# Optimization experiments

Measured on AMD Instinct MI355X. Metric: run time of the kernel, lower is better.

Reference implementation:

```python
import jax, jax.numpy as jnp
import numpy as np

E, D, H, T = 8, 1024, 2816, 16384


def setup_inputs() -> dict:
    key = jax.random.key(0)
    k1, k2, k3, k4 = jax.random.split(key, 4)
    x = jax.random.normal(k1, (T, D), dtype=jnp.float32)
    # Params sized per init (w1/w3: [E, H, D], w2: [E, D, H]), trunc-normal-ish scale 0.02
    w1 = 0.02 * jax.random.normal(k2, (E, H, D), dtype=jnp.float32)
    w2 = 0.02 * jax.random.normal(k3, (E, D, H), dtype=jnp.float32)
    w3 = 0.02 * jax.random.normal(k4, (E, H, D), dtype=jnp.float32)
    # Per-expert token counts summing to < T (tail rows are padding, output zeros)
    rng = np.random.default_rng(0)
    props = rng.dirichlet(4.0 * np.ones(E))
    counts = np.floor(props * (T - 64)).astype(np.int32)
    num_tokens_per_expert = jnp.asarray(counts, dtype=jnp.int32)
    return {"x": x, "w1": w1, "w2": w2, "w3": w3,
            "num_tokens_per_expert": num_tokens_per_expert}


def reference(x, w1, w2, w3, num_tokens_per_expert):
    # Tokens are grouped contiguously by expert; grouped GEMM via lax.ragged_dot.
    g = num_tokens_per_expert.astype(jnp.int32)
    # rhs for ragged_dot must be [groups, k, n]
    h1 = jax.lax.ragged_dot(x, jnp.swapaxes(w1, 1, 2), g)   # [T, H] = x @ w1[e].T
    h3 = jax.lax.ragged_dot(x, jnp.swapaxes(w3, 1, 2), g)   # [T, H]
    h = jax.nn.silu(h1) * h3                                # SwiGLU
    out = jax.lax.ragged_dot(h, jnp.swapaxes(w2, 1, 2), g)  # [T, D]
    # Rows beyond sum(counts) are padding -> zeros, matching torch vstack of zeros
    valid = jnp.arange(x.shape[0]) < jnp.sum(g)
    return jnp.where(valid[:, None], out, jnp.zeros((), dtype=out.dtype))
```

## Files before the change

### kernel.cpp

```cpp
#include <hip/hip_runtime.h>

#define NE 8
#define DD 1024
#define HH 2816
#define TT 16384
#define MT (TT / 128 + NE)

constexpr int NJA = MT * (HH / 128);
constexpr int NJB = MT * (DD / 128);

typedef __bf16 bf16;
typedef __bf16 bf16x4 __attribute__((ext_vector_type(4)));
typedef __bf16 bf16x8 __attribute__((ext_vector_type(8)));
typedef float f32x4 __attribute__((ext_vector_type(4)));

constexpr size_t HBUF_E = (size_t)TT * HH;
constexpr size_t XN = (size_t)TT * DD;
constexpr size_t WN = (size_t)NE * HH * DD;
constexpr size_t XB_OFF = HBUF_E * 2;
constexpr size_t W1B_OFF = XB_OFF + XN * 2;
constexpr size_t W3B_OFF = W1B_OFF + WN * 2;

__device__ __forceinline__ void gld16(const void* g, void* l) {
  __builtin_amdgcn_global_load_lds(
      (const __attribute__((address_space(1))) void*)g,
      (__attribute__((address_space(3))) void*)l, 16, 0, 0);
}

__device__ __forceinline__ f32x4 mfma16(bf16x8 a, bf16x8 b, f32x4 c) {
  return __builtin_amdgcn_mfma_f32_16x16x32_bf16(a, b, c, 0, 0, 0);
}

#define BARRIER()                      \
  do {                                 \
    __builtin_amdgcn_s_barrier();      \
    asm volatile("" ::: "memory");     \
  } while (0)

__global__ __launch_bounds__(256) void cvt_bf16_k(const float4* __restrict__ in,
                                                  bf16x4* __restrict__ out, int n4) {
  int i = blockIdx.x * 256 + threadIdx.x;
  if (i < n4) {
    float4 v = in[i];
    bf16x4 o;
    o[0] = (bf16)v.x; o[1] = (bf16)v.y; o[2] = (bf16)v.z; o[3] = (bf16)v.w;
    out[i] = o;
  }
}

struct TileInfo { int e, row0, rv; };
__device__ __forceinline__ TileInfo find_tile(const int* __restrict__ cnts, int t) {
  TileInfo ti; ti.e = -1; ti.row0 = 0; ti.rv = 0;
  int off = 0;
#pragma unroll
  for (int i = 0; i < NE; ++i) {
    int c = cnts[i];
    int tl = (c + 127) >> 7;
    if (ti.e < 0) {
      if (t < tl) {
        ti.e = i;
        ti.row0 = off + (t << 7);
        int rv = c - (t << 7);
        ti.rv = rv > 128 ? 128 : rv;
      } else {
        t -= tl;
      }
    }
    off += c;
  }
  return ti;
}

__global__ __launch_bounds__(512, 2) void swiglu_gemm_k(
    const bf16* __restrict__ x, const bf16* __restrict__ w1,
    const bf16* __restrict__ w3, const int* __restrict__ cnts,
    bf16* __restrict__ hbuf) {
  constexpr int NKT = DD / 64;

  int lin = blockIdx.x;
  lin = (lin & 7) * (NJA / 8) + (lin >> 3);
  const int tile = lin % MT;
  const int n0 = (lin / MT) * 128;
  TileInfo ti = find_tile(cnts, tile);
  if (ti.e < 0) return;

  const bf16* w1e = w1 + (size_t)ti.e * HH * DD;
  const bf16* w3e = w3 + (size_t)ti.e * HH * DD;
  const bf16* xb = x + (size_t)ti.row0 * DD;

  __shared__ bf16 sA[3][128 * 64];
  __shared__ bf16 sB1[3][128 * 64];
  __shared__ bf16 sB3[3][128 * 64];

  const int tid = threadIdx.x;
  const int lane = tid & 63, wave = tid >> 6;
  const int wm = wave >> 2, wn = wave & 3;
  const int lr = lane & 15, lkg = lane >> 4;

  const int r8 = tid >> 3;
  const int csrc = ((tid & 7) ^ (r8 & 7)) << 3;
  const int rvm1 = ti.rv - 1;
  const int ra0 = r8 > rvm1 ? rvm1 : r8;
  const int ra1 = (64 + r8) > rvm1 ? rvm1 : 64 + r8;
  const bf16* gA0 = xb + (size_t)ra0 * DD + csrc;
  const bf16* gA1 = xb + (size_t)ra1 * DD + csrc;
  const bf16* gB1a = w1e + (size_t)(n0 + r8) * DD + csrc;
  const bf16* gB1b = w1e + (size_t)(n0 + 64 + r8) * DD + csrc;
  const bf16* gB3a = w3e + (size_t)(n0 + r8) * DD + csrc;
  const bf16* gB3b = w3e + (size_t)(n0 + 64 + r8) * DD + csrc;
  const int d0 = tid * 8, d1 = 64 * 64 + tid * 8;

#define STAGE_A(kt, bb)                  \
  do {                                   \
    int kk = (kt) * 64;                  \
    gld16(gA0 + kk, &sA[bb][d0]);        \
    gld16(gA1 + kk, &sA[bb][d1]);        \
    gld16(gB1a + kk, &sB1[bb][d0]);      \
    gld16(gB1b + kk, &sB1[bb][d1]);      \
    gld16(gB3a + kk, &sB3[bb][d0]);      \
    gld16(gB3b + kk, &sB3[bb][d1]);      \
  } while (0)

  const int swz = (lkg ^ (lr & 7)) << 4;
  const int aoff = (wm * 64 + lr) * 128 + swz;
  const int boff = (wn * 32 + lr) * 128 + swz;

  f32x4 acc1[4][2], acc3[4][2];
#pragma unroll
  for (int i = 0; i < 4; ++i)
#pragma unroll
    for (int j = 0; j < 2; ++j) {
      acc1[i][j] = f32x4{0.f, 0.f, 0.f, 0.f};
      acc3[i][j] = f32x4{0.f, 0.f, 0.f, 0.f};
    }

  STAGE_A(0, 0);
  STAGE_A(1, 1);
  asm volatile("s_waitcnt vmcnt(6)" ::: "memory");
  BARRIER();

  int cur = 0;
  for (int kt = 0; kt < NKT; ++kt) {
    const bool pf = (kt + 2) < NKT;
    int nxt = cur + 2; if (nxt >= 3) nxt -= 3;
    if (pf) STAGE_A(kt + 2, nxt);

    const char* pA = (const char*)sA[cur];
    const char* pB1 = (const char*)sB1[cur];
    const char* pB3 = (const char*)sB3[cur];
    bf16x8 af[4][2], f1[2][2], f3[2][2];
#pragma unroll
    for (int mt = 0; mt < 4; ++mt)
#pragma unroll
      for (int ks = 0; ks < 2; ++ks)
        af[mt][ks] = *(const bf16x8*)(pA + ((aoff + mt * 2048) ^ (ks << 6)));
#pragma unroll
    for (int nt = 0; nt < 2; ++nt)
#pragma unroll
      for (int ks = 0; ks < 2; ++ks) {
        f1[nt][ks] = *(const bf16x8*)(pB1 + ((boff + nt * 2048) ^ (ks << 6)));
        f3[nt][ks] = *(const bf16x8*)(pB3 + ((boff + nt * 2048) ^ (ks << 6)));
      }
    __builtin_amdgcn_s_setprio(1);
#pragma unroll
    for (int ks = 0; ks < 2; ++ks)
#pragma unroll
      for (int mt = 0; mt < 4; ++mt)
#pragma unroll
        for (int nt = 0; nt < 2; ++nt) {
          acc1[mt][nt] = mfma16(af[mt][ks], f1[nt][ks], acc1[mt][nt]);
          acc3[mt][nt] = mfma16(af[mt][ks], f3[nt][ks], acc3[mt][nt]);
        }
    __builtin_amdgcn_s_setprio(0);
    if (pf) asm volatile("s_waitcnt vmcnt(6) lgkmcnt(0)" ::: "memory");
    else    asm volatile("s_waitcnt vmcnt(0) lgkmcnt(0)" ::: "memory");
    BARRIER();
    cur = (cur + 1 == 3) ? 0 : cur + 1;
  }
#undef STAGE_A

  const int rq = (lane >> 4) << 2;
#pragma unroll
  for (int mt = 0; mt < 4; ++mt)
#pragma unroll
    for (int r = 0; r < 4; ++r) {
      int row = wm * 64 + mt * 16 + rq + r;
      if (row < ti.rv) {
        size_t base = (size_t)(ti.row0 + row) * HH + n0 + wn * 32 + lr;
#pragma unroll
        for (int nt = 0; nt < 2; ++nt) {
          float a = acc1[mt][nt][r], b = acc3[mt][nt][r];
          hbuf[base + nt * 16] = (bf16)(a / (1.f + __expf(-a)) * b);
        }
      }
    }
}

__global__ __launch_bounds__(512, 2) void down_gemm_k(
    const bf16* __restrict__ hbuf, const bf16* __restrict__ w2,
    const int* __restrict__ cnts, float* __restrict__ out) {
  constexpr int NKT = HH / 64;

  int lin = blockIdx.x;
  lin = (lin & 7) * (NJB / 8) + (lin >> 3);
  const int tile = lin % MT;
  const int n0 = (lin / MT) * 128;
  TileInfo ti = find_tile(cnts, tile);
  if (ti.e < 0) return;

  const bf16* w2e = w2 + (size_t)ti.e * DD * HH;
  const bf16* hb = hbuf + (size_t)ti.row0 * HH;

  __shared__ bf16 sA[3][128 * 64];
  __shared__ bf16 sB[3][128 * 64];

  const int tid = threadIdx.x;
  const int lane = tid & 63, wave = tid >> 6;
  const int wm = wave >> 2, wn = wave & 3;
  const int lr = lane & 15, lkg = lane >> 4;

  const int r8 = tid >> 3;
  const int csrc = ((tid & 7) ^ (r8 & 7)) << 3;
  const int rvm1 = ti.rv - 1;
  const int ra0 = r8 > rvm1 ? rvm1 : r8;
  const int ra1 = (64 + r8) > rvm1 ? rvm1 : 64 + r8;
  const bf16* gA0 = hb + (size_t)ra0 * HH + csrc;
  const bf16* gA1 = hb + (size_t)ra1 * HH + csrc;
  const bf16* gBa = w2e + (size_t)(n0 + r8) * HH + csrc;
  const bf16* gBb = w2e + (size_t)(n0 + 64 + r8) * HH + csrc;
  const int d0 = tid * 8, d1 = 64 * 64 + tid * 8;

#define STAGE_B(kt, bb)                 \
  do {                                  \
    int kk = (kt) * 64;                 \
    gld16(gA0 + kk, &sA[bb][d0]);       \
    gld16(gA1 + kk, &sA[bb][d1]);       \
    gld16(gBa + kk, &sB[bb][d0]);       \
    gld16(gBb + kk, &sB[bb][d1]);       \
  } while (0)

  const int swz = (lkg ^ (lr & 7)) << 4;
  const int aoff = (wm * 64 + lr) * 128 + swz;
  const int boff = (wn * 32 + lr) * 128 + swz;

  f32x4 acc[4][2];
#pragma unroll
  for (int i = 0; i < 4; ++i)
#pragma unroll
    for (int j = 0; j < 2; ++j) acc[i][j] = f32x4{0.f, 0.f, 0.f, 0.f};

  STAGE_B(0, 0);
  STAGE_B(1, 1);
  asm volatile("s_waitcnt vmcnt(4)" ::: "memory");
  BARRIER();

  int cur = 0;
  for (int kt = 0; kt < NKT; ++kt) {
    const bool pf = (kt + 2) < NKT;
    int nxt = cur + 2; if (nxt >= 3) nxt -= 3;
    if (pf) STAGE_B(kt + 2, nxt);

    const char* pA = (const char*)sA[cur];
    const char* pB = (const char*)sB[cur];
    bf16x8 af[4][2], bfm[2][2];
#pragma unroll
    for (int mt = 0; mt < 4; ++mt)
#pragma unroll
      for (int ks = 0; ks < 2; ++ks)
        af[mt][ks] = *(const bf16x8*)(pA + ((aoff + mt * 2048) ^ (ks << 6)));
#pragma unroll
    for (int nt = 0; nt < 2; ++nt)
#pragma unroll
      for (int ks = 0; ks < 2; ++ks)
        bfm[nt][ks] = *(const bf16x8*)(pB + ((boff + nt * 2048) ^ (ks << 6)));
    __builtin_amdgcn_s_setprio(1);
#pragma unroll
    for (int ks = 0; ks < 2; ++ks)
#pragma unroll
      for (int mt = 0; mt < 4; ++mt)
#pragma unroll
        for (int nt = 0; nt < 2; ++nt)
          acc[mt][nt] = mfma16(af[mt][ks], bfm[nt][ks], acc[mt][nt]);
    __builtin_amdgcn_s_setprio(0);
    if (pf) asm volatile("s_waitcnt vmcnt(4) lgkmcnt(0)" ::: "memory");
    else    asm volatile("s_waitcnt vmcnt(0) lgkmcnt(0)" ::: "memory");
    BARRIER();
    cur = (cur + 1 == 3) ? 0 : cur + 1;
  }
#undef STAGE_B

  const int rq = (lane >> 4) << 2;
#pragma unroll
  for (int mt = 0; mt < 4; ++mt)
#pragma unroll
    for (int r = 0; r < 4; ++r) {
      int row = wm * 64 + mt * 16 + rq + r;
      if (row < ti.rv) {
        size_t base = (size_t)(ti.row0 + row) * DD + n0 + wn * 32 + lr;
#pragma unroll
        for (int nt = 0; nt < 2; ++nt) out[base + nt * 16] = acc[mt][nt][r];
      }
    }
}

extern "C" void kernel_launch(void* const* d_in, const int* in_sizes, int n_in,
                              void* d_out, int out_size, void* d_ws, size_t ws_size,
                              hipStream_t stream) {
  const float* x = (const float*)d_in[0];
  const float* w1 = (const float*)d_in[1];
  const float* w2 = (const float*)d_in[2];
  const float* w3 = (const float*)d_in[3];
  const int* cnts = (const int*)d_in[4];
  float* out = (float*)d_out;

  char* ws = (char*)d_ws;
  bf16* hbuf = (bf16*)ws;
  bf16* xb = (bf16*)(ws + XB_OFF);
  bf16* w1b = (bf16*)(ws + W1B_OFF);
  bf16* w3b = (bf16*)(ws + W3B_OFF);
  bf16* w2b = w1b;

  hipMemsetAsync(d_out, 0, (size_t)out_size * sizeof(float), stream);

  cvt_bf16_k<<<(int)(XN / 4 / 256), 256, 0, stream>>>((const float4*)x, (bf16x4*)xb, (int)(XN / 4));
  cvt_bf16_k<<<(int)(WN / 4 / 256), 256, 0, stream>>>((const float4*)w1, (bf16x4*)w1b, (int)(WN / 4));
  cvt_bf16_k<<<(int)(WN / 4 / 256), 256, 0, stream>>>((const float4*)w3, (bf16x4*)w3b, (int)(WN / 4));

  swiglu_gemm_k<<<NJA, 512, 0, stream>>>(xb, w1b, w3b, cnts, hbuf);

  cvt_bf16_k<<<(int)(WN / 4 / 256), 256, 0, stream>>>((const float4*)w2, (bf16x4*)w2b, (int)(WN / 4));

  down_gemm_k<<<NJB, 512, 0, stream>>>(hbuf, w2b, cnts, out);
}
```

Baseline: 888.2 us.

## Retile both GEMMs to 256-thread blocks with BK=32 and fuse conversions and zeroing

Both grouped GEMMs move from 512-thread blocks with a K-step of 64 to 256-thread blocks with a K-step of 32 and a smaller LDS footprint, aiming for three resident blocks per CU. The gate/up GEMM now uses 64-wide N tiles, and the down GEMM gives each wave a 64x64 sub-tile. Swapping the MFMA operands makes each lane hold four consecutive columns, so epilogue stores become vectorized (bf16x4 and f32x4). The three input conversions are merged into one launch. The full output memset is replaced by extra blocks in the down kernel that zero only the padding rows. In exchange, the K loop runs twice as many iterations, each with a barrier.

```diff
diff --git a/kernel.cpp b/kernel.cpp
--- a/kernel.cpp
+++ b/kernel.cpp
@@ -6,8 +6,9 @@
 #define TT 16384
 #define MT (TT / 128 + NE)
 
-constexpr int NJA = MT * (HH / 128);
+constexpr int NJA = MT * (HH / 64);
 constexpr int NJB = MT * (DD / 128);
+constexpr int ZBLK = 64;
 
 typedef __bf16 bf16;
 typedef __bf16 bf16x4 __attribute__((ext_vector_type(4)));
@@ -36,6 +37,29 @@
     __builtin_amdgcn_s_barrier();      \
     asm volatile("" ::: "memory");     \
   } while (0)
+
+__global__ __launch_bounds__(256) void cvt3_k(
+    const float4* __restrict__ x, const float4* __restrict__ w1,
+    const float4* __restrict__ w3, bf16x4* __restrict__ xb,
+    bf16x4* __restrict__ w1b, bf16x4* __restrict__ w3b) {
+  constexpr int NBX = (int)(XN / 4 / 256);
+  constexpr int NBW = (int)(WN / 4 / 256);
+  int b = blockIdx.x;
+  const float4* src;
+  bf16x4* dst;
+  int i;
+  if (b < NBX) {
+    src = x; dst = xb; i = b * 256 + threadIdx.x;
+  } else if (b < NBX + NBW) {
+    src = w1; dst = w1b; i = (b - NBX) * 256 + threadIdx.x;
+  } else {
+    src = w3; dst = w3b; i = (b - NBX - NBW) * 256 + threadIdx.x;
+  }
+  float4 v = src[i];
+  bf16x4 o;
+  o[0] = (bf16)v.x; o[1] = (bf16)v.y; o[2] = (bf16)v.z; o[3] = (bf16)v.w;
+  dst[i] = o;
+}
 
 __global__ __launch_bounds__(256) void cvt_bf16_k(const float4* __restrict__ in,
                                                   bf16x4* __restrict__ out, int n4) {
@@ -71,16 +95,16 @@
   return ti;
 }
 
-__global__ __launch_bounds__(512, 2) void swiglu_gemm_k(
+__global__ __launch_bounds__(256, 3) void swiglu_gemm_k(
     const bf16* __restrict__ x, const bf16* __restrict__ w1,
     const bf16* __restrict__ w3, const int* __restrict__ cnts,
     bf16* __restrict__ hbuf) {
-  constexpr int NKT = DD / 64;
+  constexpr int NKT = DD / 32;
 
   int lin = blockIdx.x;
   lin = (lin & 7) * (NJA / 8) + (lin >> 3);
   const int tile = lin % MT;
-  const int n0 = (lin / MT) * 128;
+  const int n0 = (lin / MT) * 64;
   TileInfo ti = find_tile(cnts, tile);
   if (ti.e < 0) return;
 
@@ -88,42 +112,38 @@
   const bf16* w3e = w3 + (size_t)ti.e * HH * DD;
   const bf16* xb = x + (size_t)ti.row0 * DD;
 
-  __shared__ bf16 sA[3][128 * 64];
-  __shared__ bf16 sB1[3][128 * 64];
-  __shared__ bf16 sB3[3][128 * 64];
+  __shared__ bf16 sA[3][128 * 32];
+  __shared__ bf16 sB1[3][64 * 32];
+  __shared__ bf16 sB3[3][64 * 32];
 
   const int tid = threadIdx.x;
   const int lane = tid & 63, wave = tid >> 6;
-  const int wm = wave >> 2, wn = wave & 3;
+  const int wm = wave >> 1, wn = wave & 1;
   const int lr = lane & 15, lkg = lane >> 4;
 
-  const int r8 = tid >> 3;
-  const int csrc = ((tid & 7) ^ (r8 & 7)) << 3;
+  const int r8 = tid >> 2;
+  const int csw = (((tid & 3) ^ ((r8 >> 1) & 3)) << 3);
   const int rvm1 = ti.rv - 1;
   const int ra0 = r8 > rvm1 ? rvm1 : r8;
   const int ra1 = (64 + r8) > rvm1 ? rvm1 : 64 + r8;
-  const bf16* gA0 = xb + (size_t)ra0 * DD + csrc;
-  const bf16* gA1 = xb + (size_t)ra1 * DD + csrc;
-  const bf16* gB1a = w1e + (size_t)(n0 + r8) * DD + csrc;
-  const bf16* gB1b = w1e + (size_t)(n0 + 64 + r8) * DD + csrc;
-  const bf16* gB3a = w3e + (size_t)(n0 + r8) * DD + csrc;
-  const bf16* gB3b = w3e + (size_t)(n0 + 64 + r8) * DD + csrc;
-  const int d0 = tid * 8, d1 = 64 * 64 + tid * 8;
-
-#define STAGE_A(kt, bb)                  \
-  do {                                   \
-    int kk = (kt) * 64;                  \
-    gld16(gA0 + kk, &sA[bb][d0]);        \
-    gld16(gA1 + kk, &sA[bb][d1]);        \
-    gld16(gB1a + kk, &sB1[bb][d0]);      \
-    gld16(gB1b + kk, &sB1[bb][d1]);      \
-    gld16(gB3a + kk, &sB3[bb][d0]);      \
-    gld16(gB3b + kk, &sB3[bb][d1]);      \
+  const bf16* gA0 = xb + (size_t)ra0 * DD + csw;
+  const bf16* gA1 = xb + (size_t)ra1 * DD + csw;
+  const bf16* gB1 = w1e + (size_t)(n0 + r8) * DD + csw;
+  const bf16* gB3 = w3e + (size_t)(n0 + r8) * DD + csw;
+  const int d0 = tid * 8, d1 = (256 + tid) * 8;
+
+#define STAGE_A(kt, bb)                 \
+  do {                                  \
+    int kk = (kt) * 32;                 \
+    gld16(gA0 + kk, &sA[bb][d0]);       \
+    gld16(gA1 + kk, &sA[bb][d1]);       \
+    gld16(gB1 + kk, &sB1[bb][d0]);      \
+    gld16(gB3 + kk, &sB3[bb][d0]);      \
   } while (0)
 
-  const int swz = (lkg ^ (lr & 7)) << 4;
-  const int aoff = (wm * 64 + lr) * 128 + swz;
-  const int boff = (wn * 32 + lr) * 128 + swz;
+  const int swz = (lkg ^ ((lr >> 1) & 3)) << 4;
+  const int aoff = (wm * 64 + lr) * 64 + swz;
+  const int boff = (wn * 32 + lr) * 64 + swz;
 
   f32x4 acc1[4][2], acc3[4][2];
 #pragma unroll
@@ -136,7 +156,7 @@
 
   STAGE_A(0, 0);
   STAGE_A(1, 1);
-  asm volatile("s_waitcnt vmcnt(6)" ::: "memory");
+  asm volatile("s_waitcnt vmcnt(4)" ::: "memory");
   BARRIER();
 
   int cur = 0;
@@ -148,61 +168,71 @@
     const char* pA = (const char*)sA[cur];
     const char* pB1 = (const char*)sB1[cur];
     const char* pB3 = (const char*)sB3[cur];
-    bf16x8 af[4][2], f1[2][2], f3[2][2];
+    bf16x8 af[4], f1[2], f3[2];
 #pragma unroll
     for (int mt = 0; mt < 4; ++mt)
-#pragma unroll
-      for (int ks = 0; ks < 2; ++ks)
-        af[mt][ks] = *(const bf16x8*)(pA + ((aoff + mt * 2048) ^ (ks << 6)));
-#pragma unroll
-    for (int nt = 0; nt < 2; ++nt)
-#pragma unroll
-      for (int ks = 0; ks < 2; ++ks) {
-        f1[nt][ks] = *(const bf16x8*)(pB1 + ((boff + nt * 2048) ^ (ks << 6)));
-        f3[nt][ks] = *(const bf16x8*)(pB3 + ((boff + nt * 2048) ^ (ks << 6)));
+      af[mt] = *(const bf16x8*)(pA + aoff + mt * 1024);
+#pragma unroll
+    for (int nt = 0; nt < 2; ++nt) {
+      f1[nt] = *(const bf16x8*)(pB1 + boff + nt * 1024);
+      f3[nt] = *(const bf16x8*)(pB3 + boff + nt * 1024);
+    }
+    __builtin_amdgcn_s_setprio(1);
+#pragma unroll
+    for (int mt = 0; mt < 4; ++mt)
+#pragma unroll
+      for (int nt = 0; nt < 2; ++nt) {
+        acc1[mt][nt] = mfma16(f1[nt], af[mt], acc1[mt][nt]);
+        acc3[mt][nt] = mfma16(f3[nt], af[mt], acc3[mt][nt]);
       }
-    __builtin_amdgcn_s_setprio(1);
-#pragma unroll
-    for (int ks = 0; ks < 2; ++ks)
-#pragma unroll
-      for (int mt = 0; mt < 4; ++mt)
-#pragma unroll
-        for (int nt = 0; nt < 2; ++nt) {
-          acc1[mt][nt] = mfma16(af[mt][ks], f1[nt][ks], acc1[mt][nt]);
-          acc3[mt][nt] = mfma16(af[mt][ks], f3[nt][ks], acc3[mt][nt]);
-        }
     __builtin_amdgcn_s_setprio(0);
-    if (pf) asm volatile("s_waitcnt vmcnt(6) lgkmcnt(0)" ::: "memory");
+    if (pf) asm volatile("s_waitcnt vmcnt(4) lgkmcnt(0)" ::: "memory");
     else    asm volatile("s_waitcnt vmcnt(0) lgkmcnt(0)" ::: "memory");
     BARRIER();
     cur = (cur + 1 == 3) ? 0 : cur + 1;
   }
 #undef STAGE_A
 
-  const int rq = (lane >> 4) << 2;
-#pragma unroll
-  for (int mt = 0; mt < 4; ++mt)
-#pragma unroll
-    for (int r = 0; r < 4; ++r) {
-      int row = wm * 64 + mt * 16 + rq + r;
-      if (row < ti.rv) {
-        size_t base = (size_t)(ti.row0 + row) * HH + n0 + wn * 32 + lr;
-#pragma unroll
-        for (int nt = 0; nt < 2; ++nt) {
+#pragma unroll
+  for (int mt = 0; mt < 4; ++mt) {
+    int row = wm * 64 + mt * 16 + lr;
+    if (row < ti.rv) {
+      size_t base = (size_t)(ti.row0 + row) * HH + n0 + wn * 32 + (lkg << 2);
+#pragma unroll
+      for (int nt = 0; nt < 2; ++nt) {
+        bf16x4 o;
+#pragma unroll
+        for (int r = 0; r < 4; ++r) {
           float a = acc1[mt][nt][r], b = acc3[mt][nt][r];
-          hbuf[base + nt * 16] = (bf16)(a / (1.f + __expf(-a)) * b);
+          o[r] = (bf16)(a / (1.f + __expf(-a)) * b);
         }
+        *(bf16x4*)&hbuf[base + nt * 16] = o;
       }
     }
-}
-
-__global__ __launch_bounds__(512, 2) void down_gemm_k(
+  }
+}
+
+__global__ __launch_bounds__(256, 3) void down_gemm_k(
     const bf16* __restrict__ hbuf, const bf16* __restrict__ w2,
     const int* __restrict__ cnts, float* __restrict__ out) {
-  constexpr int NKT = HH / 64;
-
-  int lin = blockIdx.x;
-  lin = (lin & 7) * (NJB / 8) + (lin >> 3);
+  constexpr int NKT = HH / 32;
+
+  int b = blockIdx.x;
+  if (b >= NJB) {
+    int total = 0;
+#pragma unroll
+    for (int e = 0; e < NE; ++e) total += cnts[e];
+    size_t base4 = (size_t)total * (DD / 4);
+    size_t n4 = ((size_t)TT * DD) / 4 - base4;
+    f32x4* o4 = (f32x4*)out + base4;
+    f32x4 z{0.f, 0.f, 0.f, 0.f};
+    for (size_t i = (size_t)(b - NJB) * 256 + threadIdx.x; i < n4;
+         i += (size_t)ZBLK * 256)
+      o4[i] = z;
+    return;
+  }
+
+  int lin = (b & 7) * (NJB / 8) + (b >> 3);
   const int tile = lin % MT;
   const int n0 = (lin / MT) * 128;
   TileInfo ti = find_tile(cnts, tile);
@@ -211,43 +241,43 @@
   const bf16* w2e = w2 + (size_t)ti.e * DD * HH;
   const bf16* hb = hbuf + (size_t)ti.row0 * HH;
 
-  __shared__ bf16 sA[3][128 * 64];
-  __shared__ bf16 sB[3][128 * 64];
+  __shared__ bf16 sA[3][128 * 32];
+  __shared__ bf16 sB[3][128 * 32];
 
   const int tid = threadIdx.x;
   const int lane = tid & 63, wave = tid >> 6;
-  const int wm = wave >> 2, wn = wave & 3;
+  const int wm = wave >> 1, wn = wave & 1;
   const int lr = lane & 15, lkg = lane >> 4;
 
-  const int r8 = tid >> 3;
-  const int csrc = ((tid & 7) ^ (r8 & 7)) << 3;
+  const int r8 = tid >> 2;
+  const int csw = (((tid & 3) ^ ((r8 >> 1) & 3)) << 3);
   const int rvm1 = ti.rv - 1;
   const int ra0 = r8 > rvm1 ? rvm1 : r8;
   const int ra1 = (64 + r8) > rvm1 ? rvm1 : 64 + r8;
-  const bf16* gA0 = hb + (size_t)ra0 * HH + csrc;
-  const bf16* gA1 = hb + (size_t)ra1 * HH + csrc;
-  const bf16* gBa = w2e + (size_t)(n0 + r8) * HH + csrc;
-  const bf16* gBb = w2e + (size_t)(n0 + 64 + r8) * HH + csrc;
-  const int d0 = tid * 8, d1 = 64 * 64 + tid * 8;
+  const bf16* gA0 = hb + (size_t)ra0 * HH + csw;
+  const bf16* gA1 = hb + (size_t)ra1 * HH + csw;
+  const bf16* gB0 = w2e + (size_t)(n0 + r8) * HH + csw;
+  const bf16* gB1 = w2e + (size_t)(n0 + 64 + r8) * HH + csw;
+  const int d0 = tid * 8, d1 = (256 + tid) * 8;
 
 #define STAGE_B(kt, bb)                 \
   do {                                  \
-    int kk = (kt) * 64;                 \
+    int kk = (kt) * 32;                 \
     gld16(gA0 + kk, &sA[bb][d0]);       \
     gld16(gA1 + kk, &sA[bb][d1]);       \
-    gld16(gBa + kk, &sB[bb][d0]);       \
-    gld16(gBb + kk, &sB[bb][d1]);       \
+    gld16(gB0 + kk, &sB[bb][d0]);       \
+    gld16(gB1 + kk, &sB[bb][d1]);       \
   } while (0)
 
-  const int swz = (lkg ^ (lr & 7)) << 4;
-  const int aoff = (wm * 64 + lr) * 128 + swz;
-  const int boff = (wn * 32 + lr) * 128 + swz;
-
-  f32x4 acc[4][2];
+  const int swz = (lkg ^ ((lr >> 1) & 3)) << 4;
+  const int aoff = (wm * 64 + lr) * 64 + swz;
+  const int boff = (wn * 64 + lr) * 64 + swz;
+
+  f32x4 acc[4][4];
 #pragma unroll
   for (int i = 0; i < 4; ++i)
 #pragma unroll
-    for (int j = 0; j < 2; ++j) acc[i][j] = f32x4{0.f, 0.f, 0.f, 0.f};
+    for (int j = 0; j < 4; ++j) acc[i][j] = f32x4{0.f, 0.f, 0.f, 0.f};
 
   STAGE_B(0, 0);
   STAGE_B(1, 1);
@@ -262,25 +292,19 @@
 
     const char* pA = (const char*)sA[cur];
     const char* pB = (const char*)sB[cur];
-    bf16x8 af[4][2], bfm[2][2];
+    bf16x8 af[4], bfm[4];
 #pragma unroll
     for (int mt = 0; mt < 4; ++mt)
-#pragma unroll
-      for (int ks = 0; ks < 2; ++ks)
-        af[mt][ks] = *(const bf16x8*)(pA + ((aoff + mt * 2048) ^ (ks << 6)));
-#pragma unroll
-    for (int nt = 0; nt < 2; ++nt)
-#pragma unroll
-      for (int ks = 0; ks < 2; ++ks)
-        bfm[nt][ks] = *(const bf16x8*)(pB + ((boff + nt * 2048) ^ (ks << 6)));
+      af[mt] = *(const bf16x8*)(pA + aoff + mt * 1024);
+#pragma unroll
+    for (int nt = 0; nt < 4; ++nt)
+      bfm[nt] = *(const bf16x8*)(pB + boff + nt * 1024);
     __builtin_amdgcn_s_setprio(1);
 #pragma unroll
-    for (int ks = 0; ks < 2; ++ks)
-#pragma unroll
-      for (int mt = 0; mt < 4; ++mt)
-#pragma unroll
-        for (int nt = 0; nt < 2; ++nt)
-          acc[mt][nt] = mfma16(af[mt][ks], bfm[nt][ks], acc[mt][nt]);
+    for (int mt = 0; mt < 4; ++mt)
+#pragma unroll
+      for (int nt = 0; nt < 4; ++nt)
+        acc[mt][nt] = mfma16(bfm[nt], af[mt], acc[mt][nt]);
     __builtin_amdgcn_s_setprio(0);
     if (pf) asm volatile("s_waitcnt vmcnt(4) lgkmcnt(0)" ::: "memory");
     else    asm volatile("s_waitcnt vmcnt(0) lgkmcnt(0)" ::: "memory");
@@ -289,18 +313,16 @@
   }
 #undef STAGE_B
 
-  const int rq = (lane >> 4) << 2;
-#pragma unroll
-  for (int mt = 0; mt < 4; ++mt)
-#pragma unroll
-    for (int r = 0; r < 4; ++r) {
-      int row = wm * 64 + mt * 16 + rq + r;
-      if (row < ti.rv) {
-        size_t base = (size_t)(ti.row0 + row) * DD + n0 + wn * 32 + lr;
-#pragma unroll
-        for (int nt = 0; nt < 2; ++nt) out[base + nt * 16] = acc[mt][nt][r];
-      }
-    }
+#pragma unroll
+  for (int mt = 0; mt < 4; ++mt) {
+    int row = wm * 64 + mt * 16 + lr;
+    if (row < ti.rv) {
+      size_t base = (size_t)(ti.row0 + row) * DD + n0 + wn * 64 + (lkg << 2);
+#pragma unroll
+      for (int nt = 0; nt < 4; ++nt)
+        *(f32x4*)&out[base + nt * 16] = acc[mt][nt];
+    }
+  }
 }
 
 extern "C" void kernel_launch(void* const* d_in, const int* in_sizes, int n_in,
@@ -320,15 +342,16 @@
   bf16* w3b = (bf16*)(ws + W3B_OFF);
   bf16* w2b = w1b;
 
-  hipMemsetAsync(d_out, 0, (size_t)out_size * sizeof(float), stream);
-
-  cvt_bf16_k<<<(int)(XN / 4 / 256), 256, 0, stream>>>((const float4*)x, (bf16x4*)xb, (int)(XN / 4));
-  cvt_bf16_k<<<(int)(WN / 4 / 256), 256, 0, stream>>>((const float4*)w1, (bf16x4*)w1b, (int)(WN / 4));
-  cvt_bf16_k<<<(int)(WN / 4 / 256), 256, 0, stream>>>((const float4*)w3, (bf16x4*)w3b, (int)(WN / 4));
-
-  swiglu_gemm_k<<<NJA, 512, 0, stream>>>(xb, w1b, w3b, cnts, hbuf);
-
-  cvt_bf16_k<<<(int)(WN / 4 / 256), 256, 0, stream>>>((const float4*)w2, (bf16x4*)w2b, (int)(WN / 4));
-
-  down_gemm_k<<<NJB, 512, 0, stream>>>(hbuf, w2b, cnts, out);
-}
+  constexpr int NBX = (int)(XN / 4 / 256);
+  constexpr int NBW = (int)(WN / 4 / 256);
+
+  cvt3_k<<<NBX + 2 * NBW, 256, 0, stream>>>((const float4*)x, (const float4*)w1,
+                                            (const float4*)w3, (bf16x4*)xb,
+                                            (bf16x4*)w1b, (bf16x4*)w3b);
+
+  swiglu_gemm_k<<<NJA, 256, 0, stream>>>(xb, w1b, w3b, cnts, hbuf);
+
+  cvt_bf16_k<<<NBW, 256, 0, stream>>>((const float4*)w2, (bf16x4*)w2b, (int)(WN / 4));
+
+  down_gemm_k<<<NJB + ZBLK, 256, 0, stream>>>(hbuf, w2b, cnts, out);
+}
```

Result: faster. 740.5 us (-16.6%).
